# Optimization experiments

Hardware: AMD Instinct MI355X
Metric: run time of the kernel (lower is better)

The kernel has to match this reference:

```python
import jax, jax.numpy as jnp
import numpy as np

B, N, D, H = 8, 1024, 1024, 16
DH = D // H
EPS = 1e-6


def setup_inputs() -> dict:
    key = jax.random.key(0)
    ks = jax.random.split(key, 12)
    s = 1.0 / np.sqrt(D)
    inp = {
        "x": jax.random.normal(ks[0], (B, N, D), jnp.float32),
        "y": jax.random.normal(ks[1], (B, N, D), jnp.float32),
        "Wq": jax.random.normal(ks[2], (D, D), jnp.float32) * s,
        "bq": jnp.zeros((D,), jnp.float32),
        "Wk": jax.random.normal(ks[3], (D, D), jnp.float32) * s,
        "bk": jnp.zeros((D,), jnp.float32),
        "Wv": jax.random.normal(ks[4], (D, D), jnp.float32) * s,
        "bv": jnp.zeros((D,), jnp.float32),
        "Wf": jax.random.normal(ks[5], (D, D), jnp.float32) * s,
        "bf": jnp.zeros((D,), jnp.float32),
        "g1": jnp.ones((D,), jnp.float32),
        "b1": jnp.zeros((D,), jnp.float32),
        "g2": jnp.ones((D,), jnp.float32),
        "b2": jnp.zeros((D,), jnp.float32),
    }
    return inp


def _layernorm(x, g, b):
    mu = jnp.mean(x, axis=-1, keepdims=True)
    var = jnp.mean(jnp.square(x - mu), axis=-1, keepdims=True)
    return (x - mu) * jax.lax.rsqrt(var + EPS) * g + b


def reference(x, y, Wq, bq, Wk, bk, Wv, bv, Wf, bf, g1, b1, g2, b2):
    q = x @ Wq + bq                      # [B, Nq, D]
    k = y @ Wk + bk                      # [B, Nk, D]
    v = y @ Wv + bv                      # [B, Nk, D]
    qh = q.reshape(B, N, H, DH)
    kh = k.reshape(B, N, H, DH)
    vh = v.reshape(B, N, H, DH)
    # NOTE: original scales by sqrt(embed_dim), not sqrt(head_dim)
    scores = jnp.einsum("bqhd,bkhd->bhqk", qh, kh) / jnp.sqrt(jnp.float32(D))
    att = jax.nn.softmax(scores, axis=-1)
    o = jnp.einsum("bhqk,bkhd->bqhd", att, vh).reshape(B, N, D)
    out = x + o
    out = _layernorm(out, g1, b1)
    out = out + jax.nn.relu(out @ Wf + bf)
    out = _layernorm(out, g2, b2)
    return out
```

## Files before the change

kernel.cpp:

```cpp
#include <hip/hip_runtime.h>


#define Bb 8
#define Nn 1024
#define Dd 1024
#define Hh 16
#define DH 64
#define Mrows (Bb * 1024)

#define QSCL 0.045084220027780106f

typedef float f32x4 __attribute__((ext_vector_type(4)));
typedef __bf16 bf16x8 __attribute__((ext_vector_type(8)));
typedef unsigned int u32x4 __attribute__((ext_vector_type(4)));

#define MFMA16(acc, a, b) \
  acc = __builtin_amdgcn_mfma_f32_16x16x32_bf16((a), (b), (acc), 0, 0, 0)

__device__ __forceinline__ bf16x8 ld_frag(const void* p) {
  u32x4 v = *(const u32x4*)p;
  return __builtin_bit_cast(bf16x8, v);
}

__device__ __forceinline__ void gload16(const void* g, void* l) {
  __builtin_amdgcn_global_load_lds(
      (const __attribute__((address_space(1))) unsigned int*)g,
      (__attribute__((address_space(3))) unsigned int*)l, 16, 0, 0);
}

__device__ __forceinline__ unsigned short f2bf(float f) {
  return __builtin_bit_cast(unsigned short, (__bf16)f);
}
__device__ __forceinline__ float bf2f(unsigned short s) {
  unsigned int u = ((unsigned int)s) << 16;
  return __builtin_bit_cast(float, u);
}
__device__ __forceinline__ unsigned cvt_pk_bf16(float a, float b) {
  unsigned r;
  asm("v_cvt_pk_bf16_f32 %0, %1, %2" : "=v"(r) : "v"(a), "v"(b));
  return r;
}

__global__ __launch_bounds__(256) void prep(
    const float* __restrict__ x, const float* __restrict__ y,
    unsigned short* __restrict__ xb, unsigned short* __restrict__ yb,
    const float* __restrict__ W0, const float* __restrict__ W1,
    const float* __restrict__ W2, const float* __restrict__ W3,
    unsigned short* __restrict__ T0, unsigned short* __restrict__ T1,
    unsigned short* __restrict__ T2, unsigned short* __restrict__ T3) {
  __shared__ float tile[32][33];
  const int z = blockIdx.z, t = threadIdx.x;
  if (z < 2) {
    const float* in = z ? y : x;
    unsigned short* out = z ? yb : xb;
    const int n4 = (Mrows * Dd) / 4;
    int i = blockIdx.x * 256 + t;
    int stride = 1024 * 256;
    for (; i < n4; i += stride) {
      float4 v = ((const float4*)in)[i];
      ushort4 o;
      o.x = f2bf(v.x); o.y = f2bf(v.y); o.z = f2bf(v.z); o.w = f2bf(v.w);
      ((ushort4*)out)[i] = o;
    }
  } else {
    const float* W = z == 2 ? W0 : z == 3 ? W1 : z == 4 ? W2 : W3;
    unsigned short* Wt = z == 2 ? T0 : z == 3 ? T1 : z == 4 ? T2 : T3;
    const int tx = t & 31, ty = t >> 5;
    const int n0 = (blockIdx.x & 31) * 32, k0 = (blockIdx.x >> 5) * 32;
#pragma unroll
    for (int i = ty; i < 32; i += 8)
      tile[i][tx] = W[(size_t)(k0 + i) * Dd + n0 + tx];
    __syncthreads();
#pragma unroll
    for (int i = ty; i < 32; i += 8)
      Wt[(size_t)(n0 + i) * Dd + k0 + tx] = f2bf(tile[tx][i]);
  }
}

struct GemmCtx { int m0, n0, wm, wn, lr, lk, lg, l, w; };

template <typename EpiFn>
__device__ __forceinline__ void gemm_core(
    const unsigned short* __restrict__ A, const unsigned short* __restrict__ Bt,
    int K, EpiFn epi) {
  __shared__ __attribute__((aligned(16))) unsigned short As[2][128 * 32];
  __shared__ __attribute__((aligned(16))) unsigned short Bs[2][128 * 32];
  const int bid = blockIdx.y * 8 + blockIdx.x;
  const int nwg = (gridDim.x * gridDim.y);
  const int swz = (bid & 7) * (nwg >> 3) + (bid >> 3);
  const int m0 = (swz >> 3) * 128, n0 = (swz & 7) * 128;
  const int t = threadIdx.x, w = t >> 6, l = t & 63;
  const int wm = (w >> 1) * 64, wn = (w & 1) * 64;
  const int lr = l & 15, lk = (l >> 4) * 8;
  const int rA = t >> 2, sA = (t & 3) * 8;
  char* AsB = (char*)As;
  char* BsB = (char*)Bs;
  const int wb = (w * 64) * 16;

  f32x4 acc[4][4] = {};

  for (int k0 = 0; k0 < K; k0 += 64) {
    __syncthreads();
#pragma unroll
    for (int h = 0; h < 2; ++h) {
      const int ko = k0 + h * 32;
      gload16(A + (size_t)(m0 + rA) * K + ko + sA, AsB + h * 8192 + wb);
      gload16(A + (size_t)(m0 + 64 + rA) * K + ko + sA, AsB + h * 8192 + wb + 4096);
      gload16(Bt + (size_t)(n0 + rA) * K + ko + sA, BsB + h * 8192 + wb);
      gload16(Bt + (size_t)(n0 + 64 + rA) * K + ko + sA, BsB + h * 8192 + wb + 4096);
    }
    __syncthreads();

#pragma unroll
    for (int h = 0; h < 2; ++h) {
      bf16x8 af[4], bfr[4];
#pragma unroll
      for (int i = 0; i < 4; ++i)
        af[i] = ld_frag(&As[h][(wm + i * 16 + lr) * 32 + lk]);
#pragma unroll
      for (int j = 0; j < 4; ++j)
        bfr[j] = ld_frag(&Bs[h][(wn + j * 16 + lr) * 32 + lk]);
#pragma unroll
      for (int i = 0; i < 4; ++i)
#pragma unroll
        for (int j = 0; j < 4; ++j) MFMA16(acc[i][j], af[i], bfr[j]);
    }
  }
  GemmCtx c{m0, n0, wm, wn, lr, lk, l >> 4, l, w};
  epi(acc, c);
}

__global__ __launch_bounds__(256) void gemm_qkv(
    const unsigned short* __restrict__ xb, const unsigned short* __restrict__ yb,
    const unsigned short* __restrict__ WqT, const unsigned short* __restrict__ WkT,
    const unsigned short* __restrict__ WvT,
    const float* __restrict__ bq, const float* __restrict__ bk,
    const float* __restrict__ bv,
    unsigned short* __restrict__ Qb, unsigned short* __restrict__ Kb,
    unsigned short* __restrict__ Vtb) {
  const int z = blockIdx.z;
  const unsigned short* A = (z == 0) ? xb : yb;
  const unsigned short* Bt = (z == 0) ? WqT : (z == 1) ? WkT : WvT;
  const float* bias = (z == 0) ? bq : (z == 1) ? bk : bv;
  unsigned short* Cb = (z == 0) ? Qb : Kb;

  gemm_core(A, Bt, Dd, [&](f32x4 (&acc)[4][4], GemmCtx c) {
#pragma unroll
    for (int i = 0; i < 4; ++i)
#pragma unroll
      for (int j = 0; j < 4; ++j) {
        int col = c.n0 + c.wn + j * 16 + c.lr;
        float bcol = bias[col];
        if (z == 2) {
          int brow = c.m0 + c.wm + i * 16 + c.lg * 4;
          int bi = brow >> 10, nloc = brow & 1023;
          int nperm = (nloc & ~31) | (((nloc >> 2) & 3) << 3) |
                      (((nloc >> 4) & 1) << 2);
          ushort4 o4;
          o4.x = f2bf(acc[i][j][0] + bcol);
          o4.y = f2bf(acc[i][j][1] + bcol);
          o4.z = f2bf(acc[i][j][2] + bcol);
          o4.w = f2bf(acc[i][j][3] + bcol);
          *(ushort4*)(Vtb + ((size_t)bi * Dd + col) * Nn + nperm) = o4;
        } else {
          float scl = (z == 0) ? QSCL : 1.0f;
#pragma unroll
          for (int r = 0; r < 4; ++r) {
            int row = c.m0 + c.wm + i * 16 + c.lg * 4 + r;
            Cb[(size_t)row * Dd + col] = f2bf((acc[i][j][r] + bcol) * scl);
          }
        }
      }
  });
}

__global__ __launch_bounds__(256) void gemm_ff(
    const unsigned short* __restrict__ A, const unsigned short* __restrict__ Bt,
    const float* __restrict__ bias, const unsigned short* __restrict__ Tres,
    unsigned short* __restrict__ Cb) {
  gemm_core(A, Bt, Dd, [&](f32x4 (&acc)[4][4], GemmCtx c) {
#pragma unroll
    for (int i = 0; i < 4; ++i)
#pragma unroll
      for (int j = 0; j < 4; ++j) {
        int col = c.n0 + c.wn + j * 16 + c.lr;
        float bcol = bias[col];
#pragma unroll
        for (int r = 0; r < 4; ++r) {
          int row = c.m0 + c.wm + i * 16 + c.lg * 4 + r;
          size_t idx = (size_t)row * Dd + col;
          Cb[idx] = f2bf(bf2f(Tres[idx]) + fmaxf(acc[i][j][r] + bcol, 0.f));
        }
      }
  });
}

__global__ __launch_bounds__(512) void attn_fwd(
    const unsigned short* __restrict__ Qg, const unsigned short* __restrict__ Kg,
    const unsigned short* __restrict__ Vt, unsigned short* __restrict__ Obf) {
  __shared__ __attribute__((aligned(16))) unsigned short KVs[2][2][64 * 64];
  char* lbase = (char*)KVs;

  const int bid = blockIdx.y * 4 + blockIdx.x;
  const int swz = (bid & 7) * 64 + (bid >> 3);
  const int q0 = (swz & 3) * 256;
  const int by = swz >> 2;
  const int b = by >> 4, h = by & 15;

  const int t = threadIdx.x, w = t >> 6, l = t & 63;
  const int lr = l & 15, lg = l >> 4;

  bf16x8 aq[2][2];
#pragma unroll
  for (int i = 0; i < 2; ++i) {
    const unsigned short* qp =
        Qg + ((size_t)b * Nn + q0 + w * 32 + i * 16 + lr) * Dd + h * DH + lg * 8;
    aq[i][0] = *(const bf16x8*)qp;
    aq[i][1] = *(const bf16x8*)(qp + 32);
  }

  u32x4 one4 = {0x3F803F80u, 0x3F803F80u, 0x3F803F80u, 0x3F803F80u};
  const bf16x8 vones = __builtin_bit_cast(bf16x8, one4);

  const size_t baseK = (size_t)b * Nn * Dd + h * DH;
  const size_t baseV = ((size_t)b * Dd + h * DH) * Nn;

  const int srow = t >> 3, sch = t & 7;
  const int sby = srow * 128 + ((sch * 16) ^ ((srow & 7) << 4));

  uint4 kA = *(const uint4*)(Kg + baseK + (size_t)srow * Dd + sch * 8);
  uint4 vA = *(const uint4*)(Vt + baseV + (size_t)srow * Nn + sch * 8);

  *(uint4*)(lbase + sby) = kA;
  *(uint4*)(lbase + 8192 + sby) = vA;
  __syncthreads();

  f32x4 oacc[4][2] = {};
  f32x4 lacc[2] = {};

  for (int kv = 0; kv < Nn / 64; ++kv) {
    char* kcur = lbase + (kv & 1) * 16384;
    char* vcur = kcur + 8192;
    const bool more = (kv + 1) < Nn / 64;
    if (more) {
      int kvo = (kv + 1) * 64;
      kA = *(const uint4*)(Kg + baseK + (size_t)(kvo + srow) * Dd + sch * 8);
      vA = *(const uint4*)(Vt + baseV + (size_t)srow * Nn + kvo + sch * 8);
    }

    f32x4 st[2][4];
    __builtin_amdgcn_s_setprio(1);
#pragma unroll
    for (int j = 0; j < 4; ++j) {
      const int kro = (j * 16 + lr) * 128;
      bf16x8 k0 = ld_frag(kcur + kro + (((lg ^ (lr & 7))) << 4));
      bf16x8 k1 = ld_frag(kcur + kro + ((((lg + 4) ^ (lr & 7))) << 4));
#pragma unroll
      for (int i = 0; i < 2; ++i) {
        f32x4 z = {0.f, 0.f, 0.f, 0.f};
        MFMA16(z, k0, aq[i][0]);
        MFMA16(z, k1, aq[i][1]);
        st[i][j] = z;
      }
    }
    __builtin_amdgcn_s_setprio(0);

#pragma unroll
    for (int i = 0; i < 2; ++i)
#pragma unroll
      for (int j = 0; j < 4; ++j) {
        st[i][j][0] = exp2f(st[i][j][0]);
        st[i][j][1] = exp2f(st[i][j][1]);
        st[i][j][2] = exp2f(st[i][j][2]);
        st[i][j][3] = exp2f(st[i][j][3]);
      }

#pragma unroll
    for (int m = 0; m < 2; ++m) {
      bf16x8 pb[2];
#pragma unroll
      for (int i = 0; i < 2; ++i) {
        u32x4 pk;
        pk[0] = cvt_pk_bf16(st[i][2 * m][0], st[i][2 * m][1]);
        pk[1] = cvt_pk_bf16(st[i][2 * m][2], st[i][2 * m][3]);
        pk[2] = cvt_pk_bf16(st[i][2 * m + 1][0], st[i][2 * m + 1][1]);
        pk[3] = cvt_pk_bf16(st[i][2 * m + 1][2], st[i][2 * m + 1][3]);
        pb[i] = __builtin_bit_cast(bf16x8, pk);
      }
      __builtin_amdgcn_s_setprio(1);
      MFMA16(lacc[0], vones, pb[0]);
      MFMA16(lacc[1], vones, pb[1]);
#pragma unroll
      for (int da = 0; da < 4; ++da) {
        const int vrow = da * 16 + lr;
        bf16x8 va = ld_frag(
            vcur + vrow * 128 + (((lg + 4 * m) ^ (vrow & 7)) << 4));
        MFMA16(oacc[da][0], va, pb[0]);
        MFMA16(oacc[da][1], va, pb[1]);
      }
      __builtin_amdgcn_s_setprio(0);
    }

    if (more) {
      char* knxt = lbase + ((kv + 1) & 1) * 16384;
      *(uint4*)(knxt + sby) = kA;
      *(uint4*)(knxt + 8192 + sby) = vA;
      __syncthreads();
    }
  }

#pragma unroll
  for (int i = 0; i < 2; ++i) {
    float rd = 1.f / lacc[i][0];
    const size_t orow = (size_t)b * Nn + q0 + w * 32 + i * 16 + lr;
#pragma unroll
    for (int da = 0; da < 4; ++da) {
      ushort4 o4;
      o4.x = f2bf(oacc[da][i][0] * rd);
      o4.y = f2bf(oacc[da][i][1] * rd);
      o4.z = f2bf(oacc[da][i][2] * rd);
      o4.w = f2bf(oacc[da][i][3] * rd);
      *(ushort4*)(Obf + orow * Dd + h * DH + da * 16 + lg * 4) = o4;
    }
  }
}

template <int MODE>
__global__ __launch_bounds__(256) void ln_k(
    const unsigned short* __restrict__ X, const unsigned short* __restrict__ Oin,
    const float* __restrict__ gamma, const float* __restrict__ beta,
    unsigned short* __restrict__ out_bf, float* __restrict__ out_f) {
  __shared__ float red[8];
  const int row = blockIdx.x, t = threadIdx.x;
  ushort4 xu = ((const ushort4*)(X + (size_t)row * Dd))[t];
  float4 v = {bf2f(xu.x), bf2f(xu.y), bf2f(xu.z), bf2f(xu.w)};
  if (MODE == 0) {
    ushort4 o = ((const ushort4*)(Oin + (size_t)row * Dd))[t];
    v.x += bf2f(o.x); v.y += bf2f(o.y); v.z += bf2f(o.z); v.w += bf2f(o.w);
  }
  float s = v.x + v.y + v.z + v.w;
#pragma unroll
  for (int o = 32; o > 0; o >>= 1) s += __shfl_xor(s, o, 64);
  if ((t & 63) == 0) red[t >> 6] = s;
  __syncthreads();
  float mean = (red[0] + red[1] + red[2] + red[3]) * (1.f / 1024.f);
  float dx = v.x - mean, dy = v.y - mean, dz = v.z - mean, dw = v.w - mean;
  float s2 = dx * dx + dy * dy + dz * dz + dw * dw;
#pragma unroll
  for (int o = 32; o > 0; o >>= 1) s2 += __shfl_xor(s2, o, 64);
  if ((t & 63) == 0) red[4 + (t >> 6)] = s2;
  __syncthreads();
  float var = (red[4] + red[5] + red[6] + red[7]) * (1.f / 1024.f);
  float rstd = rsqrtf(var + 1e-6f);
  float4 g = ((const float4*)gamma)[t];
  float4 bb = ((const float4*)beta)[t];
  float r0 = dx * rstd * g.x + bb.x;
  float r1 = dy * rstd * g.y + bb.y;
  float r2 = dz * rstd * g.z + bb.z;
  float r3 = dw * rstd * g.w + bb.w;
  if (MODE == 0) {
    ushort4 o4;
    o4.x = f2bf(r0); o4.y = f2bf(r1); o4.z = f2bf(r2); o4.w = f2bf(r3);
    ((ushort4*)(out_bf + (size_t)row * Dd))[t] = o4;
  } else {
    float4 o4 = {r0, r1, r2, r3};
    ((float4*)(out_f + (size_t)row * Dd))[t] = o4;
  }
}

extern "C" void kernel_launch(void* const* d_in, const int* in_sizes, int n_in,
                              void* d_out, int out_size, void* d_ws, size_t ws_size,
                              hipStream_t stream) {
  const float* x  = (const float*)d_in[0];
  const float* y  = (const float*)d_in[1];
  const float* Wq = (const float*)d_in[2];
  const float* bq = (const float*)d_in[3];
  const float* Wk = (const float*)d_in[4];
  const float* bk = (const float*)d_in[5];
  const float* Wv = (const float*)d_in[6];
  const float* bv = (const float*)d_in[7];
  const float* Wf = (const float*)d_in[8];
  const float* bf = (const float*)d_in[9];
  const float* g1 = (const float*)d_in[10];
  const float* b1 = (const float*)d_in[11];
  const float* g2 = (const float*)d_in[12];
  const float* b2 = (const float*)d_in[13];

  char* ws = (char*)d_ws;
  const size_t MB = 1024 * 1024;
  unsigned short* xb  = (unsigned short*)(ws + 0 * MB);
  unsigned short* yb  = (unsigned short*)(ws + 16 * MB);
  unsigned short* WqT = (unsigned short*)(ws + 32 * MB);
  unsigned short* WkT = (unsigned short*)(ws + 34 * MB);
  unsigned short* WvT = (unsigned short*)(ws + 36 * MB);
  unsigned short* WfT = (unsigned short*)(ws + 38 * MB);
  unsigned short* Qb  = (unsigned short*)(ws + 40 * MB);
  unsigned short* Kb  = (unsigned short*)(ws + 56 * MB);
  unsigned short* Vtb = (unsigned short*)(ws + 72 * MB);
  unsigned short* Obf = (unsigned short*)(ws + 16 * MB);
  unsigned short* tb  = (unsigned short*)(ws + 40 * MB);
  unsigned short* ub  = (unsigned short*)(ws + 56 * MB);

  prep<<<dim3(1024, 1, 6), 256, 0, stream>>>(
      x, y, xb, yb, Wq, Wk, Wv, Wf, WqT, WkT, WvT, WfT);

  gemm_qkv<<<dim3(8, 64, 3), 256, 0, stream>>>(
      xb, yb, WqT, WkT, WvT, bq, bk, bv, Qb, Kb, Vtb);

  attn_fwd<<<dim3(4, 128), 512, 0, stream>>>(Qb, Kb, Vtb, Obf);

  ln_k<0><<<Mrows, 256, 0, stream>>>(xb, Obf, g1, b1, tb, nullptr);

  gemm_ff<<<dim3(8, 64), 256, 0, stream>>>(tb, WfT, bf, tb, ub);

  ln_k<1><<<Mrows, 256, 0, stream>>>(ub, nullptr, g2, b2, nullptr, (float*)d_out);
}
```

Before: 195.9 us.

## Double attention query tile per block and interleave QK, exp and PV per K half

```diff
diff --git a/kernel.cpp b/kernel.cpp
--- a/kernel.cpp
+++ b/kernel.cpp
@@ -201,20 +201,20 @@
   __shared__ __attribute__((aligned(16))) unsigned short KVs[2][2][64 * 64];
   char* lbase = (char*)KVs;
 
-  const int bid = blockIdx.y * 4 + blockIdx.x;
-  const int swz = (bid & 7) * 64 + (bid >> 3);
-  const int q0 = (swz & 3) * 256;
-  const int by = swz >> 2;
+  const int bid = blockIdx.y * 2 + blockIdx.x;
+  const int swz = (bid & 7) * 32 + (bid >> 3);
+  const int q0 = (swz & 1) * 512;
+  const int by = swz >> 1;
   const int b = by >> 4, h = by & 15;
 
   const int t = threadIdx.x, w = t >> 6, l = t & 63;
   const int lr = l & 15, lg = l >> 4;
 
-  bf16x8 aq[2][2];
-#pragma unroll
-  for (int i = 0; i < 2; ++i) {
+  bf16x8 aq[4][2];
+#pragma unroll
+  for (int i = 0; i < 4; ++i) {
     const unsigned short* qp =
-        Qg + ((size_t)b * Nn + q0 + w * 32 + i * 16 + lr) * Dd + h * DH + lg * 8;
+        Qg + ((size_t)b * Nn + q0 + w * 64 + i * 16 + lr) * Dd + h * DH + lg * 8;
     aq[i][0] = *(const bf16x8*)qp;
     aq[i][1] = *(const bf16x8*)(qp + 32);
   }
@@ -235,8 +235,11 @@
   *(uint4*)(lbase + 8192 + sby) = vA;
   __syncthreads();
 
-  f32x4 oacc[4][2] = {};
-  f32x4 lacc[2] = {};
+  f32x4 oacc[4][4] = {};
+  f32x4 lacc[4] = {};
+
+  const int kx0 = ((lg ^ (lr & 7)) << 4);
+  const int kx1 = (((lg + 4) ^ (lr & 7)) << 4);
 
   for (int kv = 0; kv < Nn / 64; ++kv) {
     char* kcur = lbase + (kv & 1) * 16384;
@@ -248,55 +251,44 @@
       vA = *(const uint4*)(Vt + baseV + (size_t)srow * Nn + kvo + sch * 8);
     }
 
-    f32x4 st[2][4];
-    __builtin_amdgcn_s_setprio(1);
-#pragma unroll
-    for (int j = 0; j < 4; ++j) {
-      const int kro = (j * 16 + lr) * 128;
-      bf16x8 k0 = ld_frag(kcur + kro + (((lg ^ (lr & 7))) << 4));
-      bf16x8 k1 = ld_frag(kcur + kro + ((((lg + 4) ^ (lr & 7))) << 4));
-#pragma unroll
-      for (int i = 0; i < 2; ++i) {
-        f32x4 z = {0.f, 0.f, 0.f, 0.f};
-        MFMA16(z, k0, aq[i][0]);
-        MFMA16(z, k1, aq[i][1]);
-        st[i][j] = z;
-      }
-    }
-    __builtin_amdgcn_s_setprio(0);
-
-#pragma unroll
-    for (int i = 0; i < 2; ++i)
-#pragma unroll
-      for (int j = 0; j < 4; ++j) {
-        st[i][j][0] = exp2f(st[i][j][0]);
-        st[i][j][1] = exp2f(st[i][j][1]);
-        st[i][j][2] = exp2f(st[i][j][2]);
-        st[i][j][3] = exp2f(st[i][j][3]);
-      }
-
 #pragma unroll
     for (int m = 0; m < 2; ++m) {
-      bf16x8 pb[2];
-#pragma unroll
-      for (int i = 0; i < 2; ++i) {
+      const int kroA = ((2 * m) * 16 + lr) * 128;
+      const int kroB = ((2 * m + 1) * 16 + lr) * 128;
+      bf16x8 kf0 = ld_frag(kcur + kroA + kx0);
+      bf16x8 kf1 = ld_frag(kcur + kroA + kx1);
+      bf16x8 kf2 = ld_frag(kcur + kroB + kx0);
+      bf16x8 kf3 = ld_frag(kcur + kroB + kx1);
+
+      bf16x8 pb[4];
+#pragma unroll
+      for (int i = 0; i < 4; ++i) {
+        f32x4 z0 = {0.f, 0.f, 0.f, 0.f};
+        f32x4 z1 = {0.f, 0.f, 0.f, 0.f};
+        __builtin_amdgcn_s_setprio(1);
+        MFMA16(z0, kf0, aq[i][0]);
+        MFMA16(z0, kf1, aq[i][1]);
+        MFMA16(z1, kf2, aq[i][0]);
+        MFMA16(z1, kf3, aq[i][1]);
+        __builtin_amdgcn_s_setprio(0);
         u32x4 pk;
-        pk[0] = cvt_pk_bf16(st[i][2 * m][0], st[i][2 * m][1]);
-        pk[1] = cvt_pk_bf16(st[i][2 * m][2], st[i][2 * m][3]);
-        pk[2] = cvt_pk_bf16(st[i][2 * m + 1][0], st[i][2 * m + 1][1]);
-        pk[3] = cvt_pk_bf16(st[i][2 * m + 1][2], st[i][2 * m + 1][3]);
+        pk[0] = cvt_pk_bf16(exp2f(z0[0]), exp2f(z0[1]));
+        pk[1] = cvt_pk_bf16(exp2f(z0[2]), exp2f(z0[3]));
+        pk[2] = cvt_pk_bf16(exp2f(z1[0]), exp2f(z1[1]));
+        pk[3] = cvt_pk_bf16(exp2f(z1[2]), exp2f(z1[3]));
         pb[i] = __builtin_bit_cast(bf16x8, pk);
       }
+
       __builtin_amdgcn_s_setprio(1);
-      MFMA16(lacc[0], vones, pb[0]);
-      MFMA16(lacc[1], vones, pb[1]);
+#pragma unroll
+      for (int i = 0; i < 4; ++i) MFMA16(lacc[i], vones, pb[i]);
 #pragma unroll
       for (int da = 0; da < 4; ++da) {
         const int vrow = da * 16 + lr;
         bf16x8 va = ld_frag(
             vcur + vrow * 128 + (((lg + 4 * m) ^ (vrow & 7)) << 4));
-        MFMA16(oacc[da][0], va, pb[0]);
-        MFMA16(oacc[da][1], va, pb[1]);
+#pragma unroll
+        for (int i = 0; i < 4; ++i) MFMA16(oacc[da][i], va, pb[i]);
       }
       __builtin_amdgcn_s_setprio(0);
     }
@@ -310,9 +302,9 @@
   }
 
 #pragma unroll
-  for (int i = 0; i < 2; ++i) {
+  for (int i = 0; i < 4; ++i) {
     float rd = 1.f / lacc[i][0];
-    const size_t orow = (size_t)b * Nn + q0 + w * 32 + i * 16 + lr;
+    const size_t orow = (size_t)b * Nn + q0 + w * 64 + i * 16 + lr;
 #pragma unroll
     for (int da = 0; da < 4; ++da) {
       ushort4 o4;
@@ -407,7 +399,7 @@
   gemm_qkv<<<dim3(8, 64, 3), 256, 0, stream>>>(
       xb, yb, WqT, WkT, WvT, bq, bk, bv, Qb, Kb, Vtb);
 
-  attn_fwd<<<dim3(4, 128), 512, 0, stream>>>(Qb, Kb, Vtb, Obf);
+  attn_fwd<<<dim3(2, 128), 512, 0, stream>>>(Qb, Kb, Vtb, Obf);
 
   ln_k<0><<<Mrows, 256, 0, stream>>>(xb, Obf, g1, b1, tb, nullptr);
 
```

Result: no change. 199.1 us (+1.6%).

## Replace QKV GEMM with 256x256-tile, 8-wave, phase-pipelined kernel

Applied to the files above, without the earlier changes.

```diff
diff --git a/kernel.cpp b/kernel.cpp
--- a/kernel.cpp
+++ b/kernel.cpp
@@ -39,6 +39,14 @@
   unsigned r;
   asm("v_cvt_pk_bf16_f32 %0, %1, %2" : "=v"(r) : "v"(a), "v"(b));
   return r;
+}
+
+__device__ __forceinline__ void raw_bar() {
+  __builtin_amdgcn_sched_barrier(0);
+  asm volatile("" ::: "memory");
+  __builtin_amdgcn_s_barrier();
+  asm volatile("" ::: "memory");
+  __builtin_amdgcn_sched_barrier(0);
 }
 
 __global__ __launch_bounds__(256) void prep(
@@ -77,6 +85,145 @@
   }
 }
 
+__global__ __launch_bounds__(512, 2) void gemm_qkv256(
+    const unsigned short* __restrict__ xb, const unsigned short* __restrict__ yb,
+    const unsigned short* __restrict__ WqT, const unsigned short* __restrict__ WkT,
+    const unsigned short* __restrict__ WvT,
+    const float* __restrict__ bq, const float* __restrict__ bk,
+    const float* __restrict__ bv,
+    unsigned short* __restrict__ Qb, unsigned short* __restrict__ Kb,
+    unsigned short* __restrict__ Vtb) {
+  __shared__ __attribute__((aligned(16))) char lds[131072];
+
+  const int z = blockIdx.z;
+  const unsigned short* A = (z == 0) ? xb : yb;
+  const unsigned short* Bt = (z == 0) ? WqT : (z == 1) ? WkT : WvT;
+  const float* bias = (z == 0) ? bq : (z == 1) ? bk : bv;
+  unsigned short* Cb = (z == 0) ? Qb : Kb;
+
+  const int bid = blockIdx.y * 4 + blockIdx.x;
+  const int swz = (bid & 7) * 16 + (bid >> 3);
+  const int m0 = (swz >> 2) * 256, n0 = (swz & 3) * 256;
+
+  const int t = threadIdx.x, wid = t >> 6, l = t & 63;
+  const int wm = wid >> 2, wn = wid & 3;
+  const int lr = l & 15, lg = l >> 4;
+
+  auto stA = [&](int d, int mq, int k0) {
+#pragma unroll
+    for (int c = 0; c < 2; ++c) {
+      int rp = c * 64 + (t >> 3);
+      int grow = m0 + ((rp >> 6) << 7) + mq * 64 + (rp & 63);
+      int gch = (t & 7) ^ (rp & 7);
+      gload16(A + (size_t)grow * Dd + k0 + gch * 8,
+              lds + d * 65536 + mq * 16384 + c * 8192 + wid * 1024);
+    }
+  };
+  auto stB = [&](int d, int nq, int k0) {
+#pragma unroll
+    for (int c = 0; c < 2; ++c) {
+      int rp = c * 64 + (t >> 3);
+      int grow = n0 + ((rp >> 5) << 6) + nq * 32 + (rp & 31);
+      int gch = (t & 7) ^ (rp & 7);
+      gload16(Bt + (size_t)grow * Dd + k0 + gch * 8,
+              lds + d * 65536 + 32768 + nq * 16384 + c * 8192 + wid * 1024);
+    }
+  };
+
+  f32x4 acc[8][4] = {};
+
+  auto phase = [&](int d, int mq, int nq, auto stage, int vmMode) {
+    const char* Ab = lds + d * 65536;
+    const char* Bbse = lds + d * 65536 + 32768;
+    bf16x8 af[4][2], bfr[2][2];
+#pragma unroll
+    for (int i = 0; i < 4; ++i) {
+      int ra = mq * 128 + wm * 64 + i * 16 + lr;
+      const char* p = Ab + ra * 128;
+      int sw = (ra & 7) << 4;
+      af[i][0] = ld_frag(p + ((lg * 16) ^ sw));
+      af[i][1] = ld_frag(p + ((64 + lg * 16) ^ sw));
+    }
+#pragma unroll
+    for (int j = 0; j < 2; ++j) {
+      int rb = nq * 128 + wn * 32 + j * 16 + lr;
+      const char* p = Bbse + rb * 128;
+      int sw = (rb & 7) << 4;
+      bfr[j][0] = ld_frag(p + ((lg * 16) ^ sw));
+      bfr[j][1] = ld_frag(p + ((64 + lg * 16) ^ sw));
+    }
+    stage();
+    if (vmMode == 1) asm volatile("s_waitcnt vmcnt(4)" ::: "memory");
+    else if (vmMode == 2) asm volatile("s_waitcnt vmcnt(0)" ::: "memory");
+    __builtin_amdgcn_s_setprio(1);
+#pragma unroll
+    for (int i = 0; i < 4; ++i)
+#pragma unroll
+      for (int j = 0; j < 2; ++j) {
+        MFMA16(acc[mq * 4 + i][nq * 2 + j], af[i][0], bfr[j][0]);
+        MFMA16(acc[mq * 4 + i][nq * 2 + j], af[i][1], bfr[j][1]);
+      }
+    __builtin_amdgcn_s_setprio(0);
+    raw_bar();
+  };
+  auto nost = [&] {};
+
+  stB(0, 0, 0); stA(0, 0, 0); stB(0, 1, 0); stA(0, 1, 0);
+  stB(1, 0, 64); stA(1, 0, 64);
+  asm volatile("s_waitcnt vmcnt(4)" ::: "memory");
+  raw_bar();
+
+#pragma unroll 1
+  for (int tt = 0; tt < 7; ++tt) {
+    const int k1 = tt * 128 + 64, k2 = tt * 128 + 128, k3 = tt * 128 + 192;
+    phase(0, 0, 0, [&] { stB(1, 1, k1); }, 0);
+    phase(0, 1, 0, [&] { stA(1, 1, k1); }, 0);
+    phase(0, 0, 1, [&] { stB(0, 0, k2); }, 0);
+    phase(0, 1, 1, [&] { stA(0, 0, k2); }, 1);
+    phase(1, 0, 0, [&] { stB(0, 1, k2); }, 0);
+    phase(1, 1, 0, [&] { stA(0, 1, k2); }, 0);
+    phase(1, 0, 1, [&] { stB(1, 0, k3); }, 0);
+    phase(1, 1, 1, [&] { stA(1, 0, k3); }, 1);
+  }
+  {
+    const int k1 = 7 * 128 + 64;
+    phase(0, 0, 0, [&] { stB(1, 1, k1); }, 0);
+    phase(0, 1, 0, [&] { stA(1, 1, k1); }, 0);
+    phase(0, 0, 1, nost, 0);
+    phase(0, 1, 1, nost, 2);
+    phase(1, 0, 0, nost, 0);
+    phase(1, 1, 0, nost, 0);
+    phase(1, 0, 1, nost, 0);
+    phase(1, 1, 1, nost, 0);
+  }
+  asm volatile("s_waitcnt vmcnt(0)" ::: "memory");
+
+#pragma unroll
+  for (int i = 0; i < 8; ++i)
+#pragma unroll
+    for (int j = 0; j < 4; ++j) {
+      int col = n0 + wn * 64 + j * 16 + lr;
+      float bcol = bias[col];
+      int brow = m0 + wm * 128 + i * 16 + lg * 4;
+      if (z == 2) {
+        int bi = brow >> 10, nloc = brow & 1023;
+        int nperm = (nloc & ~31) | (((nloc >> 2) & 3) << 3) |
+                    (((nloc >> 4) & 1) << 2);
+        ushort4 o4;
+        o4.x = f2bf(acc[i][j][0] + bcol);
+        o4.y = f2bf(acc[i][j][1] + bcol);
+        o4.z = f2bf(acc[i][j][2] + bcol);
+        o4.w = f2bf(acc[i][j][3] + bcol);
+        *(ushort4*)(Vtb + ((size_t)bi * Dd + col) * Nn + nperm) = o4;
+      } else {
+        float scl = (z == 0) ? QSCL : 1.0f;
+#pragma unroll
+        for (int r = 0; r < 4; ++r)
+          Cb[(size_t)(brow + r) * Dd + col] = f2bf((acc[i][j][r] + bcol) * scl);
+      }
+    }
+}
+
 struct GemmCtx { int m0, n0, wm, wn, lr, lk, lg, l, w; };
 
 template <typename EpiFn>
@@ -130,50 +277,6 @@
   epi(acc, c);
 }
 
-__global__ __launch_bounds__(256) void gemm_qkv(
-    const unsigned short* __restrict__ xb, const unsigned short* __restrict__ yb,
-    const unsigned short* __restrict__ WqT, const unsigned short* __restrict__ WkT,
-    const unsigned short* __restrict__ WvT,
-    const float* __restrict__ bq, const float* __restrict__ bk,
-    const float* __restrict__ bv,
-    unsigned short* __restrict__ Qb, unsigned short* __restrict__ Kb,
-    unsigned short* __restrict__ Vtb) {
-  const int z = blockIdx.z;
-  const unsigned short* A = (z == 0) ? xb : yb;
-  const unsigned short* Bt = (z == 0) ? WqT : (z == 1) ? WkT : WvT;
-  const float* bias = (z == 0) ? bq : (z == 1) ? bk : bv;
-  unsigned short* Cb = (z == 0) ? Qb : Kb;
-
-  gemm_core(A, Bt, Dd, [&](f32x4 (&acc)[4][4], GemmCtx c) {
-#pragma unroll
-    for (int i = 0; i < 4; ++i)
-#pragma unroll
-      for (int j = 0; j < 4; ++j) {
-        int col = c.n0 + c.wn + j * 16 + c.lr;
-        float bcol = bias[col];
-        if (z == 2) {
-          int brow = c.m0 + c.wm + i * 16 + c.lg * 4;
-          int bi = brow >> 10, nloc = brow & 1023;
-          int nperm = (nloc & ~31) | (((nloc >> 2) & 3) << 3) |
-                      (((nloc >> 4) & 1) << 2);
-          ushort4 o4;
-          o4.x = f2bf(acc[i][j][0] + bcol);
-          o4.y = f2bf(acc[i][j][1] + bcol);
-          o4.z = f2bf(acc[i][j][2] + bcol);
-          o4.w = f2bf(acc[i][j][3] + bcol);
-          *(ushort4*)(Vtb + ((size_t)bi * Dd + col) * Nn + nperm) = o4;
-        } else {
-          float scl = (z == 0) ? QSCL : 1.0f;
-#pragma unroll
-          for (int r = 0; r < 4; ++r) {
-            int row = c.m0 + c.wm + i * 16 + c.lg * 4 + r;
-            Cb[(size_t)row * Dd + col] = f2bf((acc[i][j][r] + bcol) * scl);
-          }
-        }
-      }
-  });
-}
-
 __global__ __launch_bounds__(256) void gemm_ff(
     const unsigned short* __restrict__ A, const unsigned short* __restrict__ Bt,
     const float* __restrict__ bias, const unsigned short* __restrict__ Tres,
@@ -257,10 +360,10 @@
       bf16x8 k1 = ld_frag(kcur + kro + ((((lg + 4) ^ (lr & 7))) << 4));
 #pragma unroll
       for (int i = 0; i < 2; ++i) {
-        f32x4 z = {0.f, 0.f, 0.f, 0.f};
-        MFMA16(z, k0, aq[i][0]);
-        MFMA16(z, k1, aq[i][1]);
-        st[i][j] = z;
+        f32x4 zz = {0.f, 0.f, 0.f, 0.f};
+        MFMA16(zz, k0, aq[i][0]);
+        MFMA16(zz, k1, aq[i][1]);
+        st[i][j] = zz;
       }
     }
     __builtin_amdgcn_s_setprio(0);
@@ -404,7 +507,7 @@
   prep<<<dim3(1024, 1, 6), 256, 0, stream>>>(
       x, y, xb, yb, Wq, Wk, Wv, Wf, WqT, WkT, WvT, WfT);
 
-  gemm_qkv<<<dim3(8, 64, 3), 256, 0, stream>>>(
+  gemm_qkv256<<<dim3(4, 32, 3), 512, 0, stream>>>(
       xb, yb, WqT, WkT, WvT, bq, bk, bv, Qb, Kb, Vtb);
 
   attn_fwd<<<dim3(4, 128), 512, 0, stream>>>(Qb, Kb, Vtb, Obf);
```

New measurement: 201.3 us. 2.7% more time.

## Fuse K and V projections into one GEMM sharing the y tile

Applied to the files above, without the earlier changes.

```diff
diff --git a/kernel.cpp b/kernel.cpp
--- a/kernel.cpp
+++ b/kernel.cpp
@@ -130,48 +130,116 @@
   epi(acc, c);
 }
 
-__global__ __launch_bounds__(256) void gemm_qkv(
-    const unsigned short* __restrict__ xb, const unsigned short* __restrict__ yb,
-    const unsigned short* __restrict__ WqT, const unsigned short* __restrict__ WkT,
-    const unsigned short* __restrict__ WvT,
-    const float* __restrict__ bq, const float* __restrict__ bk,
-    const float* __restrict__ bv,
-    unsigned short* __restrict__ Qb, unsigned short* __restrict__ Kb,
-    unsigned short* __restrict__ Vtb) {
-  const int z = blockIdx.z;
-  const unsigned short* A = (z == 0) ? xb : yb;
-  const unsigned short* Bt = (z == 0) ? WqT : (z == 1) ? WkT : WvT;
-  const float* bias = (z == 0) ? bq : (z == 1) ? bk : bv;
-  unsigned short* Cb = (z == 0) ? Qb : Kb;
-
-  gemm_core(A, Bt, Dd, [&](f32x4 (&acc)[4][4], GemmCtx c) {
+__global__ __launch_bounds__(256) void gemm_q(
+    const unsigned short* __restrict__ xb, const unsigned short* __restrict__ WqT,
+    const float* __restrict__ bqp, unsigned short* __restrict__ Qb) {
+  gemm_core(xb, WqT, Dd, [&](f32x4 (&acc)[4][4], GemmCtx c) {
 #pragma unroll
     for (int i = 0; i < 4; ++i)
 #pragma unroll
       for (int j = 0; j < 4; ++j) {
         int col = c.n0 + c.wn + j * 16 + c.lr;
-        float bcol = bias[col];
-        if (z == 2) {
-          int brow = c.m0 + c.wm + i * 16 + c.lg * 4;
-          int bi = brow >> 10, nloc = brow & 1023;
-          int nperm = (nloc & ~31) | (((nloc >> 2) & 3) << 3) |
-                      (((nloc >> 4) & 1) << 2);
-          ushort4 o4;
-          o4.x = f2bf(acc[i][j][0] + bcol);
-          o4.y = f2bf(acc[i][j][1] + bcol);
-          o4.z = f2bf(acc[i][j][2] + bcol);
-          o4.w = f2bf(acc[i][j][3] + bcol);
-          *(ushort4*)(Vtb + ((size_t)bi * Dd + col) * Nn + nperm) = o4;
-        } else {
-          float scl = (z == 0) ? QSCL : 1.0f;
-#pragma unroll
-          for (int r = 0; r < 4; ++r) {
-            int row = c.m0 + c.wm + i * 16 + c.lg * 4 + r;
-            Cb[(size_t)row * Dd + col] = f2bf((acc[i][j][r] + bcol) * scl);
-          }
+        float bcol = bqp[col];
+#pragma unroll
+        for (int r = 0; r < 4; ++r) {
+          int row = c.m0 + c.wm + i * 16 + c.lg * 4 + r;
+          Qb[(size_t)row * Dd + col] = f2bf((acc[i][j][r] + bcol) * QSCL);
         }
       }
   });
+}
+
+__global__ __launch_bounds__(256) void gemm_kv(
+    const unsigned short* __restrict__ yb,
+    const unsigned short* __restrict__ WkT, const unsigned short* __restrict__ WvT,
+    const float* __restrict__ bkp, const float* __restrict__ bvp,
+    unsigned short* __restrict__ Kb, unsigned short* __restrict__ Vtb) {
+  __shared__ __attribute__((aligned(16))) unsigned short As[2][128 * 32];
+  __shared__ __attribute__((aligned(16))) unsigned short BsK[2][128 * 32];
+  __shared__ __attribute__((aligned(16))) unsigned short BsV[2][128 * 32];
+  const int bid = blockIdx.y * 8 + blockIdx.x;
+  const int nwg = (gridDim.x * gridDim.y);
+  const int swz = (bid & 7) * (nwg >> 3) + (bid >> 3);
+  const int m0 = (swz >> 3) * 128, n0 = (swz & 7) * 128;
+  const int t = threadIdx.x, w = t >> 6, l = t & 63;
+  const int wm = (w >> 1) * 64, wn = (w & 1) * 64;
+  const int lr = l & 15, lk = (l >> 4) * 8;
+  const int rA = t >> 2, sA = (t & 3) * 8;
+  char* AsB = (char*)As;
+  char* BKB = (char*)BsK;
+  char* BVB = (char*)BsV;
+  const int wb = (w * 64) * 16;
+
+  f32x4 accK[4][4] = {};
+  f32x4 accV[4][4] = {};
+
+  for (int k0 = 0; k0 < Dd; k0 += 64) {
+    __syncthreads();
+#pragma unroll
+    for (int h = 0; h < 2; ++h) {
+      const int ko = k0 + h * 32;
+      gload16(yb + (size_t)(m0 + rA) * Dd + ko + sA, AsB + h * 8192 + wb);
+      gload16(yb + (size_t)(m0 + 64 + rA) * Dd + ko + sA, AsB + h * 8192 + wb + 4096);
+      gload16(WkT + (size_t)(n0 + rA) * Dd + ko + sA, BKB + h * 8192 + wb);
+      gload16(WkT + (size_t)(n0 + 64 + rA) * Dd + ko + sA, BKB + h * 8192 + wb + 4096);
+      gload16(WvT + (size_t)(n0 + rA) * Dd + ko + sA, BVB + h * 8192 + wb);
+      gload16(WvT + (size_t)(n0 + 64 + rA) * Dd + ko + sA, BVB + h * 8192 + wb + 4096);
+    }
+    __syncthreads();
+
+#pragma unroll
+    for (int h = 0; h < 2; ++h) {
+      bf16x8 af[4];
+#pragma unroll
+      for (int i = 0; i < 4; ++i)
+        af[i] = ld_frag(&As[h][(wm + i * 16 + lr) * 32 + lk]);
+      {
+        bf16x8 bfr[4];
+#pragma unroll
+        for (int j = 0; j < 4; ++j)
+          bfr[j] = ld_frag(&BsK[h][(wn + j * 16 + lr) * 32 + lk]);
+#pragma unroll
+        for (int i = 0; i < 4; ++i)
+#pragma unroll
+          for (int j = 0; j < 4; ++j) MFMA16(accK[i][j], af[i], bfr[j]);
+      }
+      {
+        bf16x8 bfr[4];
+#pragma unroll
+        for (int j = 0; j < 4; ++j)
+          bfr[j] = ld_frag(&BsV[h][(wn + j * 16 + lr) * 32 + lk]);
+#pragma unroll
+        for (int i = 0; i < 4; ++i)
+#pragma unroll
+          for (int j = 0; j < 4; ++j) MFMA16(accV[i][j], af[i], bfr[j]);
+      }
+    }
+  }
+
+  const int lg = l >> 4;
+#pragma unroll
+  for (int i = 0; i < 4; ++i)
+#pragma unroll
+    for (int j = 0; j < 4; ++j) {
+      int col = n0 + wn + j * 16 + lr;
+      float bcK = bkp[col];
+#pragma unroll
+      for (int r = 0; r < 4; ++r) {
+        int row = m0 + wm + i * 16 + lg * 4 + r;
+        Kb[(size_t)row * Dd + col] = f2bf(accK[i][j][r] + bcK);
+      }
+      float bcV = bvp[col];
+      int brow = m0 + wm + i * 16 + lg * 4;
+      int bi = brow >> 10, nloc = brow & 1023;
+      int nperm = (nloc & ~31) | (((nloc >> 2) & 3) << 3) |
+                  (((nloc >> 4) & 1) << 2);
+      ushort4 o4;
+      o4.x = f2bf(accV[i][j][0] + bcV);
+      o4.y = f2bf(accV[i][j][1] + bcV);
+      o4.z = f2bf(accV[i][j][2] + bcV);
+      o4.w = f2bf(accV[i][j][3] + bcV);
+      *(ushort4*)(Vtb + ((size_t)bi * Dd + col) * Nn + nperm) = o4;
+    }
 }
 
 __global__ __launch_bounds__(256) void gemm_ff(
@@ -257,10 +325,10 @@
       bf16x8 k1 = ld_frag(kcur + kro + ((((lg + 4) ^ (lr & 7))) << 4));
 #pragma unroll
       for (int i = 0; i < 2; ++i) {
-        f32x4 z = {0.f, 0.f, 0.f, 0.f};
-        MFMA16(z, k0, aq[i][0]);
-        MFMA16(z, k1, aq[i][1]);
-        st[i][j] = z;
+        f32x4 zz = {0.f, 0.f, 0.f, 0.f};
+        MFMA16(zz, k0, aq[i][0]);
+        MFMA16(zz, k1, aq[i][1]);
+        st[i][j] = zz;
       }
     }
     __builtin_amdgcn_s_setprio(0);
@@ -404,8 +472,8 @@
   prep<<<dim3(1024, 1, 6), 256, 0, stream>>>(
       x, y, xb, yb, Wq, Wk, Wv, Wf, WqT, WkT, WvT, WfT);
 
-  gemm_qkv<<<dim3(8, 64, 3), 256, 0, stream>>>(
-      xb, yb, WqT, WkT, WvT, bq, bk, bv, Qb, Kb, Vtb);
+  gemm_kv<<<dim3(8, 64), 256, 0, stream>>>(yb, WkT, WvT, bk, bv, Kb, Vtb);
+  gemm_q<<<dim3(8, 64), 256, 0, stream>>>(xb, WqT, bq, Qb);
 
   attn_fwd<<<dim3(4, 128), 512, 0, stream>>>(Qb, Kb, Vtb, Obf);
 
```

After: 226.5 us. 1.16x slower.
